# Kernel optimization log

Measured on AMD Instinct MI355X. Metric: run time of the kernel, lower is better.

The kernel has to match this reference:

```python
import jax, jax.numpy as jnp
import numpy as np

GATE_INIT_BIAS = -0.6931471805599453  # -log(2)

def mish(x):
    return x * jnp.tanh(jax.nn.softplus(x))

def setup_inputs() -> dict:
    key = jax.random.key(0)
    ks = jax.random.split(key, 24)
    B = 262144
    x = jax.random.normal(ks[0], (B, 18), dtype=jnp.float32)
    band = jax.random.randint(ks[1], (B,), 0, 9).astype(jnp.float32)
    x = x.at[:, 17].set(band)
    def lin(k, fan_in, shape):
        bound = 1.0 / np.sqrt(fan_in)
        return jax.random.uniform(k, shape, jnp.float32, -bound, bound)
    inp = {
        'x': x,
        # trunk: 15->512->256 (Mish)
        'tw1': lin(ks[2], 15, (15, 512)),  'tb1': lin(ks[3], 15, (512,)),
        'tw2': lin(ks[4], 512, (512, 256)), 'tb2': lin(ks[5], 512, (256,)),
        # 9 band heads: 256->128->1, stacked on leading axis
        'hw1': lin(ks[6], 256, (9, 256, 128)), 'hb1': lin(ks[7], 256, (9, 128)),
        'hw2': lin(ks[8], 128, (9, 128)),      'hb2': lin(ks[9], 128, (9,)),
        # sun scaler head 256->64->1 (final layer zero weight, bias = gate_init_bias)
        'sw1': lin(ks[10], 256, (256, 64)), 'sb1': lin(ks[11], 256, (64,)),
        'sw2': jnp.zeros((64, 1), jnp.float32), 'sb2': jnp.full((1,), GATE_INIT_BIAS, jnp.float32),
        # storm scaler head
        'stw1': lin(ks[12], 256, (256, 64)), 'stb1': lin(ks[13], 256, (64,)),
        'stw2': jnp.zeros((64, 1), jnp.float32), 'stb2': jnp.full((1,), GATE_INIT_BIAS, jnp.float32),
        # monotonic sidecars: 1->8->1, softplus-positivized weights
        'sun_w1': lin(ks[14], 1, (1, 8)),  'sun_b1': lin(ks[15], 1, (8,)),
        'sun_w2': lin(ks[16], 8, (8, 1)),  'sun_b2': lin(ks[17], 8, (1,)),
        'storm_w1': lin(ks[18], 1, (1, 8)), 'storm_b1': lin(ks[19], 1, (8,)),
        'storm_w2': lin(ks[20], 8, (8, 1)), 'storm_b2': lin(ks[21], 8, (1,)),
    }
    return inp

def monotonic_mlp(v, w1, b1, w2, b2):
    # MonotonicMLP: positivity via softplus on weights, tanh hidden activation
    h = jnp.tanh(v @ jax.nn.softplus(w1) + b1)
    return h @ jax.nn.softplus(w2) + b2  # [B,1]

def reference(x, tw1, tb1, tw2, tb2, hw1, hb1, hw2, hb2,
              sw1, sb1, sw2, sb2, stw1, stb1, stw2, stb2,
              sun_w1, sun_b1, sun_w2, sun_b2,
              storm_w1, storm_b1, storm_w2, storm_b2):
    x_deep = x[:, :15]
    x_sfi = x[:, 15:16]
    x_kp = x[:, 16:17]
    band = x[:, 17].astype(jnp.int32)  # [B]

    # trunk
    t = mish(mish(x_deep @ tw1 + tb1) @ tw2 + tb2)  # [B,256]

    # all 9 band heads densely (faithful to original), then gather
    hh = mish(jnp.einsum('bd,kdh->bkh', t, hw1) + hb1)       # [B,9,128]
    all_heads = jnp.einsum('bkh,kh->bk', hh, hw2) + hb2      # [B,9]
    base_snr = jnp.take_along_axis(all_heads, band[:, None], axis=1)  # [B,1]

    sun_logit = mish(t @ sw1 + sb1) @ sw2 + sb2      # [B,1]
    storm_logit = mish(t @ stw1 + stb1) @ stw2 + stb2
    sun_gate = jax.nn.sigmoid(sun_logit)
    storm_gate = jax.nn.sigmoid(storm_logit)

    return base_snr + sun_gate * monotonic_mlp(x_sfi, sun_w1, sun_b1, sun_w2, sun_b2) \
                    + storm_gate * monotonic_mlp(x_kp, storm_w1, storm_b1, storm_w2, storm_b2)
```

## Files before the change

kernel.cpp:

```cpp
#include <hip/hip_runtime.h>
#include <cstdint>

typedef unsigned short u16;
typedef unsigned char u8;
typedef __attribute__((ext_vector_type(8))) __bf16 bf16x8;
typedef __attribute__((ext_vector_type(4))) float f32x4;
typedef __attribute__((ext_vector_type(2))) unsigned u32x2;

#define MFMA16(a, b, c) __builtin_amdgcn_mfma_f32_16x16x32_bf16((a), (b), (c), 0, 0, 0)

__device__ __forceinline__ u16 f2b(float f) {
    union { float f; unsigned u; } v; v.f = f;
    unsigned r = v.u + 0x7fffu + ((v.u >> 16) & 1u);
    return (u16)(r >> 16);
}
__device__ __forceinline__ u16 f2b_hw(float f) {
    union { __bf16 h; u16 u; } cv; cv.h = (__bf16)f; return cv.u;
}
__device__ __forceinline__ float b2f(u16 h) {
    union { unsigned u; float f; } v; v.u = ((unsigned)h) << 16; return v.f;
}
__device__ __forceinline__ unsigned cvt_pk_bf16(float lo, float hi) {
    unsigned r;
    asm("v_cvt_pk_bf16_f32 %0, %1, %2" : "=v"(r) : "v"(lo), "v"(hi));
    return r;
}
__device__ __forceinline__ float fast_rcp(float x) { return __builtin_amdgcn_rcpf(x); }
__device__ __forceinline__ float mish_f(float x) {
    float s = __expf(fminf(x, 40.0f));
    float p = s * (s + 2.0f);
    return x * p * fast_rcp(p + 2.0f);
}
__device__ __forceinline__ float tanh_f(float y) {
    float e = __expf(2.0f * y);
    return 1.0f - 2.0f * fast_rcp(e + 1.0f);
}
__device__ __forceinline__ float sigmoid_f(float y) {
    return fast_rcp(1.0f + __expf(-y));
}
__device__ __forceinline__ float splus(float w) { return log1pf(__expf(w)); }


template <int CTRL>
__device__ __forceinline__ float dpp_add(float v) {
    union { float f; int i; } s, p;
    s.f = v;
    p.i = __builtin_amdgcn_update_dpp(0, s.i, CTRL, 0xf, 0xf, true);
    return v + p.f;
}

#define WS_PERM      0u
#define WS_CNT       1179648u
#define WS_SP        1191936u
#define WS_W1P       1192064u
#define WS_W2F       1224832u
#define WS_HW1F      1486976u
#define WS_SWF       2076800u
#define WS_STWF      2109568u
#define WS_NEEDED    2142336u

#define GFLAG_IDX    2336
#define NSUB         8
#define CAPH         4096
#define REG_BLOCKS   64


__global__ __launch_bounds__(512) void k_pack(const float* __restrict__ x, int B,
                       const float* __restrict__ tw1, const float* __restrict__ tw2,
                       const float* __restrict__ hw1,
                       const float* __restrict__ sw1, const float* __restrict__ stw1,
                       const float* __restrict__ sw2, const float* __restrict__ stw2,
                       const float* __restrict__ sun_w1, const float* __restrict__ sun_w2,
                       const float* __restrict__ storm_w1, const float* __restrict__ storm_w2,
                       u16* __restrict__ W1p, u16* __restrict__ W2f, u16* __restrict__ HWf,
                       u16* __restrict__ SWf, u16* __restrict__ STWf,
                       float* __restrict__ sp, int* __restrict__ cnt,
                       int* __restrict__ perm)
{
    __shared__ int wcnt[8][9];
    __shared__ int wpre[8][9];
    __shared__ int bbase[9];
    __shared__ u8 bL[512];
    const int tid  = threadIdx.x;
    const int lane = tid & 63, wave = tid >> 6;
    const int sub  = blockIdx.x & (NSUB - 1);
    const int i    = blockIdx.x * 512 + tid;

    {
        const size_t ebase = (size_t)blockIdx.x * 512 * 18;
        const float2* xs = (const float2*)(x + ebase);
        const size_t etotal = (size_t)B * 18;
        for (int p = tid; p < 4608; p += 512) {
            if (ebase + (size_t)p * 2 + 1 < etotal) {
                float2 v = xs[p];
                int e0 = p * 2;
                int r0 = e0 / 18, c0 = e0 - r0 * 18;
                if (c0 == 16) bL[r0] = (u8)(int)v.y;
            }
        }
    }
    __syncthreads();

    int band = -1, rank = 0;
    if (i < B) band = (int)bL[tid];
    for (int k = 0; k < 9; ++k) {
        unsigned long long m = __ballot(band == k);
        if (band == k) rank = __popcll(m & ((1ull << lane) - 1ull));
        if (lane == 0) wcnt[wave][k] = __popcll(m);
    }
    __syncthreads();
    if (tid < 9) {
        int run = 0;
        for (int w = 0; w < 8; ++w) { wpre[w][tid] = run; run += wcnt[w][tid]; }
        bbase[tid] = atomicAdd(&cnt[(tid * NSUB + sub) * 32], run);
    }
    __syncthreads();
    if (band >= 0)
        perm[(band * NSUB + sub) * CAPH + bbase[band] + wpre[wave][band] + rank] = i;

    if (blockIdx.x == 0 && tid < 64) {
        bool z = (sw2[tid] == 0.0f) && (stw2[tid] == 0.0f);
        unsigned long long m = __ballot(z);
        if (tid == 0) cnt[GFLAG_IDX] = (m == ~0ull) ? 1 : 0;
    }

    const int gtid = blockIdx.x * 512 + tid;
    if (gtid < 32) {
        const float* srcs[4] = { sun_w1, sun_w2, storm_w1, storm_w2 };
        float w = srcs[gtid >> 3][gtid & 7];
        sp[gtid] = splus(w);
    }
    const int total = 16384 + 131072 + 294912 + 16384 + 16384;
    for (int i2 = gtid; i2 < total; i2 += 512 * 512) {
        int idx = i2;
        if (idx < 16384) {
            int n = idx >> 5, k = idx & 31;
            W1p[idx] = (k < 15) ? f2b(tw1[k * 512 + n]) : (u16)0;
        } else if ((idx -= 16384) < 131072) {
            int tile = idx >> 9, within = idx & 511;
            int lane2 = within >> 3, j = within & 7;
            int nt = tile >> 4, kb = tile & 15;
            int n = nt * 16 + (lane2 & 15);
            int k = kb * 32 + (lane2 >> 4) * 8 + j;
            W2f[idx] = f2b(tw2[k * 256 + n]);
        } else if ((idx -= 131072) < 294912) {
            int g = idx >> 15, r = idx & 32767;
            int tile = r >> 9, within = r & 511;
            int lane2 = within >> 3, j = within & 7;
            int nt = tile >> 3, kb = tile & 7;
            int n = nt * 16 + (lane2 & 15);
            int k = kb * 32 + (lane2 >> 4) * 8 + j;
            HWf[idx] = f2b(hw1[(g * 256 + k) * 128 + n]);
        } else if ((idx -= 294912) < 16384) {
            int tile = idx >> 9, within = idx & 511;
            int lane2 = within >> 3, j = within & 7;
            int nt = tile >> 3, kb = tile & 7;
            int n = nt * 16 + (lane2 & 15);
            int k = kb * 32 + (lane2 >> 4) * 8 + j;
            SWf[idx] = f2b(sw1[k * 64 + n]);
        } else {
            idx -= 16384;
            int tile = idx >> 9, within = idx & 511;
            int lane2 = within >> 3, j = within & 7;
            int nt = tile >> 3, kb = tile & 7;
            int n = nt * 16 + (lane2 & 15);
            int k = kb * 32 + (lane2 >> 4) * 8 + j;
            STWf[idx] = f2b(stw1[k * 64 + n]);
        }
    }
}

__global__ __launch_bounds__(512, 4) void k_main(
                       const float* __restrict__ x,
                       const int* __restrict__ perm,
                       const int* __restrict__ cnt,
                       const u16* __restrict__ W1p, const u16* __restrict__ W2f,
                       const u16* __restrict__ HWf,
                       const u16* __restrict__ SWf, const u16* __restrict__ STWf,
                       const float* __restrict__ tb1, const float* __restrict__ tb2,
                       const float* __restrict__ hb1, const float* __restrict__ hw2,
                       const float* __restrict__ hb2,
                       const float* __restrict__ sb1, const float* __restrict__ sw2,
                       const float* __restrict__ sb2,
                       const float* __restrict__ stb1, const float* __restrict__ stw2,
                       const float* __restrict__ stb2,
                       const float* __restrict__ sp,
                       const float* __restrict__ sun_b1, const float* __restrict__ sun_b2,
                       const float* __restrict__ storm_b1, const float* __restrict__ storm_b2,
                       float* __restrict__ out)
{
    const int region = blockIdx.x >> 6;
    const int loc    = blockIdx.x & 63;
    const int bb     = region >> 3;
    const int nr0    = cnt[region * 32] - loc * 64;
    if (nr0 <= 0) return;
    const int nrows  = nr0 > 64 ? 64 : nr0;
    const int rstart = region * CAPH + loc * 64;
    const int gskip  = cnt[GFLAG_IDX];

    __shared__ union {
        u16 xA[64][32];
        float red[16][64];
    } su;
    __shared__ int rowsL[64];
    __shared__ float sfiL[64], kpL[64];
    __shared__ u16 buf[2][64][136];

    int tid = threadIdx.x;
    int lane = tid & 63, wave = tid >> 6;
    int quad = lane >> 4, l15 = lane & 15;

    if (tid < 64) {
        int r = rstart + (tid < nrows ? tid : 0);
        rowsL[tid] = perm[r];
    }
    for (int i = tid; i < 64 * 32; i += 512) ((u16*)su.xA)[i] = 0;
    __syncthreads();
    for (int i = tid; i < 64 * 18; i += 512) {
        int r = i / 18, c = i - r * 18;
        float v = x[rowsL[r] * 18 + c];
        if (c < 15) su.xA[r][c] = f2b_hw(v);
        else if (c == 15) sfiL[r] = v;
        else if (c == 16) kpL[r] = v;
    }
    __syncthreads();

    bf16x8 ax[4];
#pragma unroll
    for (int mt = 0; mt < 4; ++mt)
        ax[mt] = *(const bf16x8*)&su.xA[mt * 16 + l15][quad * 8];

    f32x4 acc2[2][4] = {};

    for (int c = 0; c < 4; ++c) {
        f32x4 acc1[4] = {};
        {
            int ncol = c * 128 + wave * 16 + l15;
            bf16x8 bw = *(const bf16x8*)&W1p[ncol * 32 + quad * 8];
#pragma unroll
            for (int mt = 0; mt < 4; ++mt)
                acc1[mt] = MFMA16(bw, ax[mt], acc1[mt]);
        }
        u16 (*bufc)[136] = buf[c & 1];
        {
            const f32x4 bias = *(const f32x4*)&tb1[c * 128 + wave * 16 + quad * 4];
#pragma unroll
            for (int mt = 0; mt < 4; ++mt) {
                u32x2 pk;
                pk.x = cvt_pk_bf16(mish_f(acc1[mt][0] + bias[0]),
                                   mish_f(acc1[mt][1] + bias[1]));
                pk.y = cvt_pk_bf16(mish_f(acc1[mt][2] + bias[2]),
                                   mish_f(acc1[mt][3] + bias[3]));
                *(u32x2*)&bufc[mt * 16 + l15][wave * 16 + quad * 4] = pk;
            }
        }
        __syncthreads();
        for (int ks = 0; ks < 4; ++ks) {
            bf16x8 a2[4];
#pragma unroll
            for (int mt = 0; mt < 4; ++mt)
                a2[mt] = *(const bf16x8*)&bufc[mt * 16 + l15][ks * 32 + quad * 8];
            int kb = c * 4 + ks;
#pragma unroll
            for (int ntl = 0; ntl < 2; ++ntl) {
                int nt = wave * 2 + ntl;
                bf16x8 bw = *(const bf16x8*)&W2f[((nt * 16 + kb) << 9) + lane * 8];
#pragma unroll
                for (int mt = 0; mt < 4; ++mt)
                    acc2[ntl][mt] = MFMA16(bw, a2[mt], acc2[ntl][mt]);
            }
        }
    }
    __syncthreads();

    u16 (*tmat)[264] = (u16(*)[264])buf;
#pragma unroll
    for (int ntl = 0; ntl < 2; ++ntl) {
        const int colb = wave * 32 + ntl * 16 + quad * 4;
        const f32x4 bias = *(const f32x4*)&tb2[colb];
#pragma unroll
        for (int mt = 0; mt < 4; ++mt) {
            u32x2 pk;
            pk.x = cvt_pk_bf16(mish_f(acc2[ntl][mt][0] + bias[0]),
                               mish_f(acc2[ntl][mt][1] + bias[1]));
            pk.y = cvt_pk_bf16(mish_f(acc2[ntl][mt][2] + bias[2]),
                               mish_f(acc2[ntl][mt][3] + bias[3]));
            *(u32x2*)&tmat[mt * 16 + l15][colb] = pk;
        }
    }
    __syncthreads();

    f32x4 acch[4] = {}, accg[4] = {};
    const u16* Hw = HWf + bb * 32768;
    const u16* Gw = (wave < 4) ? SWf : STWf;
    int gnt = wave & 3;
    for (int kb = 0; kb < 8; ++kb) {
        bf16x8 a3[4];
#pragma unroll
        for (int mt = 0; mt < 4; ++mt)
            a3[mt] = *(const bf16x8*)&tmat[mt * 16 + l15][kb * 32 + quad * 8];
        bf16x8 bh = *(const bf16x8*)&Hw[((wave * 8 + kb) << 9) + lane * 8];
#pragma unroll
        for (int mt = 0; mt < 4; ++mt)
            acch[mt] = MFMA16(bh, a3[mt], acch[mt]);
        if (!gskip) {
            bf16x8 bg = *(const bf16x8*)&Gw[((gnt * 8 + kb) << 9) + lane * 8];
#pragma unroll
            for (int mt = 0; mt < 4; ++mt)
                accg[mt] = MFMA16(bg, a3[mt], accg[mt]);
        }
    }

    float hpart[4], gpart[4];
    {
        const int colb = wave * 16 + quad * 4;
        const f32x4 hb = *(const f32x4*)&hb1[bb * 128 + colb];
        const f32x4 wv = *(const f32x4*)&hw2[bb * 128 + colb];
#pragma unroll
        for (int mt = 0; mt < 4; ++mt) {
            float s = mish_f(acch[mt][0] + hb[0]) * wv[0];
            s += mish_f(acch[mt][1] + hb[1]) * wv[1];
            s += mish_f(acch[mt][2] + hb[2]) * wv[2];
            s += mish_f(acch[mt][3] + hb[3]) * wv[3];
            hpart[mt] = s;
        }
    }
    if (!gskip) {
        const int nb = gnt * 16 + quad * 4;
        const f32x4 gb = (wave < 4) ? *(const f32x4*)&sb1[nb] : *(const f32x4*)&stb1[nb];
        const f32x4 gw = (wave < 4) ? *(const f32x4*)&sw2[nb] : *(const f32x4*)&stw2[nb];
#pragma unroll
        for (int mt = 0; mt < 4; ++mt) {
            float s = mish_f(accg[mt][0] + gb[0]) * gw[0];
            s += mish_f(accg[mt][1] + gb[1]) * gw[1];
            s += mish_f(accg[mt][2] + gb[2]) * gw[2];
            s += mish_f(accg[mt][3] + gb[3]) * gw[3];
            gpart[mt] = s;
        }
    }
#pragma unroll
    for (int mt = 0; mt < 4; ++mt) {
        float h = hpart[mt];
        h += __shfl_xor(h, 16); h += __shfl_xor(h, 32);
        if (quad == 0) su.red[wave][mt * 16 + l15] = h;
        if (!gskip) {
            float g = gpart[mt];
            g += __shfl_xor(g, 16); g += __shfl_xor(g, 32);
            if (quad == 0) su.red[8 + wave][mt * 16 + l15] = g;
        }
    }
    __syncthreads();

    if (tid < 64 && tid < nrows) {
        int row = tid;
        float head = hb2[bb];
#pragma unroll
        for (int w = 0; w < 8; ++w) head += su.red[w][row];
        float sl = sb2[0], tl = stb2[0];
        if (!gskip) {
#pragma unroll
            for (int w = 0; w < 4; ++w) { sl += su.red[8 + w][row]; tl += su.red[12 + w][row]; }
        }
        float sg = sigmoid_f(sl);
        float tg = sigmoid_f(tl);
        float v1 = sfiL[row], v2 = kpL[row];
        float sun_val = sun_b2[0], storm_val = storm_b2[0];
#pragma unroll
        for (int j = 0; j < 8; ++j) {
            sun_val   += tanh_f(v1 * sp[j]      + sun_b1[j])   * sp[8 + j];
            storm_val += tanh_f(v2 * sp[16 + j] + storm_b1[j]) * sp[24 + j];
        }
        out[rowsL[row]] = head + sg * sun_val + tg * storm_val;
    }
}

__global__ __launch_bounds__(64) void k_simple(
    const float* __restrict__ x,
    const float* __restrict__ tw1, const float* __restrict__ tb1,
    const float* __restrict__ tw2, const float* __restrict__ tb2,
    const float* __restrict__ hw1, const float* __restrict__ hb1,
    const float* __restrict__ hw2, const float* __restrict__ hb2,
    const float* __restrict__ sw1, const float* __restrict__ sb1,
    const float* __restrict__ sw2, const float* __restrict__ sb2,
    const float* __restrict__ stw1, const float* __restrict__ stb1,
    const float* __restrict__ stw2, const float* __restrict__ stb2,
    const float* __restrict__ sun_w1, const float* __restrict__ sun_b1,
    const float* __restrict__ sun_w2, const float* __restrict__ sun_b2,
    const float* __restrict__ storm_w1, const float* __restrict__ storm_b1,
    const float* __restrict__ storm_w2, const float* __restrict__ storm_b2,
    float* __restrict__ out)
{
    __shared__ u16 t_lds[256 * 64];

    const int lane = threadIdx.x;
    const int r = blockIdx.x * 64 + lane;

    float xr[15];
#pragma unroll
    for (int k = 0; k < 15; ++k) xr[k] = x[r * 18 + k];
    const float sfi = x[r * 18 + 15];
    const float kp  = x[r * 18 + 16];
    const int band  = (int)x[r * 18 + 17];

    for (int tc = 0; tc < 4; ++tc) {
        float acc[64];
#pragma unroll
        for (int j = 0; j < 64; ++j) acc[j] = 0.0f;
        for (int n = 0; n < 512; ++n) {
            float p = tb1[n];
#pragma unroll
            for (int k = 0; k < 15; ++k) p += xr[k] * tw1[k * 512 + n];
            const float a1n = mish_f(p);
            const float* w2 = &tw2[n * 256 + tc * 64];
#pragma unroll
            for (int j = 0; j < 64; ++j) acc[j] += a1n * w2[j];
        }
#pragma unroll
        for (int j = 0; j < 64; ++j)
            t_lds[(tc * 64 + j) * 64 + lane] = f2b(mish_f(acc[j] + tb2[tc * 64 + j]));
    }
    __syncthreads();

    float head_val = 0.0f;
    for (int g = 0; g < 9; ++g) {
        float hs = 0.0f;
        for (int hc = 0; hc < 2; ++hc) {
            float pre[64];
#pragma unroll
            for (int j = 0; j < 64; ++j) pre[j] = 0.0f;
            for (int d = 0; d < 256; ++d) {
                const float td = b2f(t_lds[d * 64 + lane]);
                const float* wv = &hw1[g * 32768 + d * 128 + hc * 64];
#pragma unroll
                for (int j = 0; j < 64; ++j) pre[j] += td * wv[j];
            }
#pragma unroll
            for (int j = 0; j < 64; ++j) {
                const int h = hc * 64 + j;
                hs += mish_f(pre[j] + hb1[g * 128 + h]) * hw2[g * 128 + h];
            }
        }
        head_val += (band == g) ? (hs + hb2[g]) : 0.0f;
    }

    float pre_s[64], pre_t[64];
#pragma unroll
    for (int j = 0; j < 64; ++j) { pre_s[j] = 0.0f; pre_t[j] = 0.0f; }
    for (int d = 0; d < 256; ++d) {
        const float td = b2f(t_lds[d * 64 + lane]);
        const float* ws1 = &sw1[d * 64];
        const float* wt1 = &stw1[d * 64];
#pragma unroll
        for (int j = 0; j < 64; ++j) {
            pre_s[j] += td * ws1[j];
            pre_t[j] += td * wt1[j];
        }
    }
    float ls = sb2[0], lt = stb2[0];
#pragma unroll
    for (int j = 0; j < 64; ++j) {
        ls += mish_f(pre_s[j] + sb1[j]) * sw2[j];
        lt += mish_f(pre_t[j] + stb1[j]) * stw2[j];
    }
    const float sg = sigmoid_f(ls);
    const float tg = sigmoid_f(lt);

    float sun_val = sun_b2[0], storm_val = storm_b2[0];
#pragma unroll
    for (int j = 0; j < 8; ++j) {
        sun_val   += tanh_f(sfi * splus(sun_w1[j])  + sun_b1[j])   * splus(sun_w2[j]);
        storm_val += tanh_f(kp * splus(storm_w1[j]) + storm_b1[j]) * splus(storm_w2[j]);
    }

    out[r] = head_val + sg * sun_val + tg * storm_val;
}

extern "C" void kernel_launch(void* const* d_in, const int* in_sizes, int n_in,
                              void* d_out, int out_size, void* d_ws, size_t ws_size,
                              hipStream_t stream) {
    (void)n_in; (void)out_size;
    const float* x        = (const float*)d_in[0];
    const float* tw1      = (const float*)d_in[1];
    const float* tb1      = (const float*)d_in[2];
    const float* tw2      = (const float*)d_in[3];
    const float* tb2      = (const float*)d_in[4];
    const float* hw1      = (const float*)d_in[5];
    const float* hb1      = (const float*)d_in[6];
    const float* hw2      = (const float*)d_in[7];
    const float* hb2      = (const float*)d_in[8];
    const float* sw1      = (const float*)d_in[9];
    const float* sb1      = (const float*)d_in[10];
    const float* sw2      = (const float*)d_in[11];
    const float* sb2      = (const float*)d_in[12];
    const float* stw1     = (const float*)d_in[13];
    const float* stb1     = (const float*)d_in[14];
    const float* stw2     = (const float*)d_in[15];
    const float* stb2     = (const float*)d_in[16];
    const float* sun_w1   = (const float*)d_in[17];
    const float* sun_b1   = (const float*)d_in[18];
    const float* sun_w2   = (const float*)d_in[19];
    const float* sun_b2   = (const float*)d_in[20];
    const float* storm_w1 = (const float*)d_in[21];
    const float* storm_b1 = (const float*)d_in[22];
    const float* storm_w2 = (const float*)d_in[23];
    const float* storm_b2 = (const float*)d_in[24];

    const int B = in_sizes[0] / 18;

    if (ws_size < (size_t)WS_NEEDED) {
        k_simple<<<B / 64, 64, 0, stream>>>(x, tw1, tb1, tw2, tb2, hw1, hb1, hw2, hb2,
                                            sw1, sb1, sw2, sb2, stw1, stb1, stw2, stb2,
                                            sun_w1, sun_b1, sun_w2, sun_b2,
                                            storm_w1, storm_b1, storm_w2, storm_b2,
                                            (float*)d_out);
        return;
    }

    char* ws = (char*)d_ws;
    int*   perm      = (int*)(ws + WS_PERM);
    int*   cnt       = (int*)(ws + WS_CNT);
    float* sp        = (float*)(ws + WS_SP);
    u16*   W1p       = (u16*)(ws + WS_W1P);
    u16*   W2f       = (u16*)(ws + WS_W2F);
    u16*   HWf       = (u16*)(ws + WS_HW1F);
    u16*   SWf       = (u16*)(ws + WS_SWF);
    u16*   STWf      = (u16*)(ws + WS_STWF);

    hipMemsetAsync(cnt, 0, 72 * 32 * sizeof(int), stream);
    k_pack<<<(B + 511) / 512, 512, 0, stream>>>(x, B, tw1, tw2, hw1, sw1, stw1,
                                                sw2, stw2,
                                                sun_w1, sun_w2, storm_w1, storm_w2,
                                                W1p, W2f, HWf, SWf, STWf, sp, cnt, perm);
    k_main<<<72 * REG_BLOCKS, 512, 0, stream>>>(x, perm, cnt,
                                                W1p, W2f, HWf, SWf, STWf,
                                                tb1, tb2, hb1, hw2, hb2,
                                                sb1, sw2, sb2, stb1, stw2, stb2,
                                                sp, sun_b1, sun_b2, storm_b1, storm_b2,
                                                (float*)d_out);
}
```

Baseline: 279.3 us.

## Software-pipeline trunk layer-1 chunks against layer-2 MFMAs and fold biases into accumulators

Computes the first trunk layer chunk before the loop, then inside each chunk iteration issues the next chunk's layer-1 MFMAs and Mish between the two halves of the layer-2 MFMAs. It writes the result into the other LDS buffer, so each chunk needs only one barrier. Biases for all layers are now loaded as initial accumulator values instead of being added before each Mish, and the zeroing loop stores 32-bit words. This is meant to hide transcendental and LDS latency behind matrix work and trim some VALU adds, at the cost of more live registers, which may lower occupancy.

```diff
diff --git a/kernel.cpp b/kernel.cpp
--- a/kernel.cpp
+++ b/kernel.cpp
@@ -214,7 +214,7 @@
         int r = rstart + (tid < nrows ? tid : 0);
         rowsL[tid] = perm[r];
     }
-    for (int i = tid; i < 64 * 32; i += 512) ((u16*)su.xA)[i] = 0;
+    for (int i = tid; i < 64 * 16; i += 512) ((unsigned*)su.xA)[i] = 0u;
     __syncthreads();
     for (int i = tid; i < 64 * 18; i += 512) {
         int r = i / 18, c = i - r * 18;
@@ -230,32 +230,46 @@
     for (int mt = 0; mt < 4; ++mt)
         ax[mt] = *(const bf16x8*)&su.xA[mt * 16 + l15][quad * 8];
 
-    f32x4 acc2[2][4] = {};
-
+    const int colq = wave * 16 + quad * 4;
+
+    f32x4 acc2[2][4];
+#pragma unroll
+    for (int ntl = 0; ntl < 2; ++ntl) {
+        const f32x4 b2v = *(const f32x4*)&tb2[wave * 32 + ntl * 16 + quad * 4];
+#pragma unroll
+        for (int mt = 0; mt < 4; ++mt) acc2[ntl][mt] = b2v;
+    }
+
+    {
+        const f32x4 b1v = *(const f32x4*)&tb1[colq];
+        bf16x8 bw = *(const bf16x8*)&W1p[(wave * 16 + l15) * 32 + quad * 8];
+        f32x4 acc1[4];
+#pragma unroll
+        for (int mt = 0; mt < 4; ++mt) { acc1[mt] = b1v; acc1[mt] = MFMA16(bw, ax[mt], acc1[mt]); }
+#pragma unroll
+        for (int mt = 0; mt < 4; ++mt) {
+            u32x2 pk;
+            pk.x = cvt_pk_bf16(mish_f(acc1[mt][0]), mish_f(acc1[mt][1]));
+            pk.y = cvt_pk_bf16(mish_f(acc1[mt][2]), mish_f(acc1[mt][3]));
+            *(u32x2*)&buf[0][mt * 16 + l15][colq] = pk;
+        }
+    }
+    __syncthreads();
+
+#pragma unroll
     for (int c = 0; c < 4; ++c) {
-        f32x4 acc1[4] = {};
-        {
-            int ncol = c * 128 + wave * 16 + l15;
-            bf16x8 bw = *(const bf16x8*)&W1p[ncol * 32 + quad * 8];
-#pragma unroll
-            for (int mt = 0; mt < 4; ++mt)
-                acc1[mt] = MFMA16(bw, ax[mt], acc1[mt]);
-        }
         u16 (*bufc)[136] = buf[c & 1];
-        {
-            const f32x4 bias = *(const f32x4*)&tb1[c * 128 + wave * 16 + quad * 4];
-#pragma unroll
-            for (int mt = 0; mt < 4; ++mt) {
-                u32x2 pk;
-                pk.x = cvt_pk_bf16(mish_f(acc1[mt][0] + bias[0]),
-                                   mish_f(acc1[mt][1] + bias[1]));
-                pk.y = cvt_pk_bf16(mish_f(acc1[mt][2] + bias[2]),
-                                   mish_f(acc1[mt][3] + bias[3]));
-                *(u32x2*)&bufc[mt * 16 + l15][wave * 16 + quad * 4] = pk;
-            }
-        }
-        __syncthreads();
-        for (int ks = 0; ks < 4; ++ks) {
+        u16 (*bufn)[136] = buf[(c + 1) & 1];
+
+        bf16x8 bwn;
+        f32x4 b1vn;
+        if (c < 3) {
+            b1vn = *(const f32x4*)&tb1[(c + 1) * 128 + colq];
+            bwn = *(const bf16x8*)&W1p[((c + 1) * 128 + wave * 16 + l15) * 32 + quad * 8];
+        }
+
+#pragma unroll
+        for (int ks = 0; ks < 2; ++ks) {
             bf16x8 a2[4];
 #pragma unroll
             for (int mt = 0; mt < 4; ++mt)
@@ -270,30 +284,72 @@
                     acc2[ntl][mt] = MFMA16(bw, a2[mt], acc2[ntl][mt]);
             }
         }
-    }
-    __syncthreads();
+
+        f32x4 acc1n[4];
+        if (c < 3) {
+#pragma unroll
+            for (int mt = 0; mt < 4; ++mt) { acc1n[mt] = b1vn; acc1n[mt] = MFMA16(bwn, ax[mt], acc1n[mt]); }
+        }
+
+#pragma unroll
+        for (int ks = 2; ks < 4; ++ks) {
+            bf16x8 a2[4];
+#pragma unroll
+            for (int mt = 0; mt < 4; ++mt)
+                a2[mt] = *(const bf16x8*)&bufc[mt * 16 + l15][ks * 32 + quad * 8];
+            int kb = c * 4 + ks;
+#pragma unroll
+            for (int ntl = 0; ntl < 2; ++ntl) {
+                int nt = wave * 2 + ntl;
+                bf16x8 bw = *(const bf16x8*)&W2f[((nt * 16 + kb) << 9) + lane * 8];
+#pragma unroll
+                for (int mt = 0; mt < 4; ++mt)
+                    acc2[ntl][mt] = MFMA16(bw, a2[mt], acc2[ntl][mt]);
+            }
+        }
+
+        if (c < 3) {
+#pragma unroll
+            for (int mt = 0; mt < 4; ++mt) {
+                u32x2 pk;
+                pk.x = cvt_pk_bf16(mish_f(acc1n[mt][0]), mish_f(acc1n[mt][1]));
+                pk.y = cvt_pk_bf16(mish_f(acc1n[mt][2]), mish_f(acc1n[mt][3]));
+                *(u32x2*)&bufn[mt * 16 + l15][colq] = pk;
+            }
+        }
+        __syncthreads();
+    }
 
     u16 (*tmat)[264] = (u16(*)[264])buf;
 #pragma unroll
     for (int ntl = 0; ntl < 2; ++ntl) {
         const int colb = wave * 32 + ntl * 16 + quad * 4;
-        const f32x4 bias = *(const f32x4*)&tb2[colb];
 #pragma unroll
         for (int mt = 0; mt < 4; ++mt) {
             u32x2 pk;
-            pk.x = cvt_pk_bf16(mish_f(acc2[ntl][mt][0] + bias[0]),
-                               mish_f(acc2[ntl][mt][1] + bias[1]));
-            pk.y = cvt_pk_bf16(mish_f(acc2[ntl][mt][2] + bias[2]),
-                               mish_f(acc2[ntl][mt][3] + bias[3]));
+            pk.x = cvt_pk_bf16(mish_f(acc2[ntl][mt][0]), mish_f(acc2[ntl][mt][1]));
+            pk.y = cvt_pk_bf16(mish_f(acc2[ntl][mt][2]), mish_f(acc2[ntl][mt][3]));
             *(u32x2*)&tmat[mt * 16 + l15][colb] = pk;
         }
     }
     __syncthreads();
 
-    f32x4 acch[4] = {}, accg[4] = {};
     const u16* Hw = HWf + bb * 32768;
     const u16* Gw = (wave < 4) ? SWf : STWf;
     int gnt = wave & 3;
+    f32x4 acch[4], accg[4];
+    const f32x4 hb = *(const f32x4*)&hb1[bb * 128 + colq];
+#pragma unroll
+    for (int mt = 0; mt < 4; ++mt) acch[mt] = hb;
+    if (!gskip) {
+        const int nb = gnt * 16 + quad * 4;
+        const f32x4 gb = (wave < 4) ? *(const f32x4*)&sb1[nb] : *(const f32x4*)&stb1[nb];
+#pragma unroll
+        for (int mt = 0; mt < 4; ++mt) accg[mt] = gb;
+    } else {
+#pragma unroll
+        for (int mt = 0; mt < 4; ++mt) accg[mt] = (f32x4){0.f, 0.f, 0.f, 0.f};
+    }
     for (int kb = 0; kb < 8; ++kb) {
         bf16x8 a3[4];
 #pragma unroll
@@ -313,28 +369,25 @@
 
     float hpart[4], gpart[4];
     {
-        const int colb = wave * 16 + quad * 4;
-        const f32x4 hb = *(const f32x4*)&hb1[bb * 128 + colb];
-        const f32x4 wv = *(const f32x4*)&hw2[bb * 128 + colb];
+        const f32x4 wv = *(const f32x4*)&hw2[bb * 128 + colq];
 #pragma unroll
         for (int mt = 0; mt < 4; ++mt) {
-            float s = mish_f(acch[mt][0] + hb[0]) * wv[0];
-            s += mish_f(acch[mt][1] + hb[1]) * wv[1];
-            s += mish_f(acch[mt][2] + hb[2]) * wv[2];
-            s += mish_f(acch[mt][3] + hb[3]) * wv[3];
+            float s = mish_f(acch[mt][0]) * wv[0];
+            s += mish_f(acch[mt][1]) * wv[1];
+            s += mish_f(acch[mt][2]) * wv[2];
+            s += mish_f(acch[mt][3]) * wv[3];
             hpart[mt] = s;
         }
     }
     if (!gskip) {
         const int nb = gnt * 16 + quad * 4;
-        const f32x4 gb = (wave < 4) ? *(const f32x4*)&sb1[nb] : *(const f32x4*)&stb1[nb];
         const f32x4 gw = (wave < 4) ? *(const f32x4*)&sw2[nb] : *(const f32x4*)&stw2[nb];
 #pragma unroll
         for (int mt = 0; mt < 4; ++mt) {
-            float s = mish_f(accg[mt][0] + gb[0]) * gw[0];
-            s += mish_f(accg[mt][1] + gb[1]) * gw[1];
-            s += mish_f(accg[mt][2] + gb[2]) * gw[2];
-            s += mish_f(accg[mt][3] + gb[3]) * gw[3];
+            float s = mish_f(accg[mt][0]) * gw[0];
+            s += mish_f(accg[mt][1]) * gw[1];
+            s += mish_f(accg[mt][2]) * gw[2];
+            s += mish_f(accg[mt][3]) * gw[3];
             gpart[mt] = s;
         }
     }
```

Result: no change. 282.8 us (+1.2%).

## Double rows per block to 128 and fold biases into MFMA accumulators

Applied to the files above, without the earlier changes.

Each block now processes 128 rows instead of 64, with half as many blocks per region, so every weight fragment loaded from global memory feeds eight MFMAs instead of four. Bias vectors now initialise the accumulators, which removes the separate bias adds before each Mish. The wave reductions are also written into the per-row reduction buffer directly. In exchange, registers and LDS per block roughly double (buf grows to about 70KB), which may lower occupancy, and partially filled tail blocks waste more work.

```diff
diff --git a/kernel.cpp b/kernel.cpp
--- a/kernel.cpp
+++ b/kernel.cpp
@@ -62,7 +62,8 @@
 #define GFLAG_IDX    2336
 #define NSUB         8
 #define CAPH         4096
-#define REG_BLOCKS   64
+#define ROWS_PB      128
+#define REG_BLOCKS   32
 
 
 __global__ __launch_bounds__(512) void k_pack(const float* __restrict__ x, int B,
@@ -189,34 +190,34 @@
                        const float* __restrict__ storm_b1, const float* __restrict__ storm_b2,
                        float* __restrict__ out)
 {
-    const int region = blockIdx.x >> 6;
-    const int loc    = blockIdx.x & 63;
+    const int region = blockIdx.x >> 5;
+    const int loc    = blockIdx.x & 31;
     const int bb     = region >> 3;
-    const int nr0    = cnt[region * 32] - loc * 64;
+    const int nr0    = cnt[region * 32] - loc * ROWS_PB;
     if (nr0 <= 0) return;
-    const int nrows  = nr0 > 64 ? 64 : nr0;
-    const int rstart = region * CAPH + loc * 64;
+    const int nrows  = nr0 > ROWS_PB ? ROWS_PB : nr0;
+    const int rstart = region * CAPH + loc * ROWS_PB;
     const int gskip  = cnt[GFLAG_IDX];
 
     __shared__ union {
-        u16 xA[64][32];
-        float red[16][64];
+        u16 xA[128][32];
+        float red[16][128];
     } su;
-    __shared__ int rowsL[64];
-    __shared__ float sfiL[64], kpL[64];
-    __shared__ u16 buf[2][64][136];
+    __shared__ int rowsL[128];
+    __shared__ float sfiL[128], kpL[128];
+    __shared__ u16 buf[2][128][136];
 
     int tid = threadIdx.x;
     int lane = tid & 63, wave = tid >> 6;
     int quad = lane >> 4, l15 = lane & 15;
 
-    if (tid < 64) {
+    if (tid < 128) {
         int r = rstart + (tid < nrows ? tid : 0);
         rowsL[tid] = perm[r];
     }
-    for (int i = tid; i < 64 * 32; i += 512) ((u16*)su.xA)[i] = 0;
-    __syncthreads();
-    for (int i = tid; i < 64 * 18; i += 512) {
+    for (int i = tid; i < 128 * 16; i += 512) ((unsigned*)su.xA)[i] = 0u;
+    __syncthreads();
+    for (int i = tid; i < 128 * 18; i += 512) {
         int r = i / 18, c = i - r * 18;
         float v = x[rowsL[r] * 18 + c];
         if (c < 15) su.xA[r][c] = f2b_hw(v);
@@ -225,40 +226,38 @@
     }
     __syncthreads();
 
-    bf16x8 ax[4];
-#pragma unroll
-    for (int mt = 0; mt < 4; ++mt)
-        ax[mt] = *(const bf16x8*)&su.xA[mt * 16 + l15][quad * 8];
-
-    f32x4 acc2[2][4] = {};
+    const int colq = wave * 16 + quad * 4;
+
+    f32x4 acc2[2][8];
+#pragma unroll
+    for (int ntl = 0; ntl < 2; ++ntl) {
+        const f32x4 b2v = *(const f32x4*)&tb2[wave * 32 + ntl * 16 + quad * 4];
+#pragma unroll
+        for (int mt = 0; mt < 8; ++mt) acc2[ntl][mt] = b2v;
+    }
 
     for (int c = 0; c < 4; ++c) {
-        f32x4 acc1[4] = {};
-        {
-            int ncol = c * 128 + wave * 16 + l15;
-            bf16x8 bw = *(const bf16x8*)&W1p[ncol * 32 + quad * 8];
-#pragma unroll
-            for (int mt = 0; mt < 4; ++mt)
-                acc1[mt] = MFMA16(bw, ax[mt], acc1[mt]);
-        }
         u16 (*bufc)[136] = buf[c & 1];
         {
-            const f32x4 bias = *(const f32x4*)&tb1[c * 128 + wave * 16 + quad * 4];
-#pragma unroll
-            for (int mt = 0; mt < 4; ++mt) {
+            const f32x4 b1v = *(const f32x4*)&tb1[c * 128 + colq];
+            bf16x8 bw = *(const bf16x8*)&W1p[(c * 128 + wave * 16 + l15) * 32 + quad * 8];
+#pragma unroll
+            for (int mt = 0; mt < 8; ++mt) {
+                bf16x8 ax = *(const bf16x8*)&su.xA[mt * 16 + l15][quad * 8];
+                f32x4 a1 = b1v;
+                a1 = MFMA16(bw, ax, a1);
                 u32x2 pk;
-                pk.x = cvt_pk_bf16(mish_f(acc1[mt][0] + bias[0]),
-                                   mish_f(acc1[mt][1] + bias[1]));
-                pk.y = cvt_pk_bf16(mish_f(acc1[mt][2] + bias[2]),
-                                   mish_f(acc1[mt][3] + bias[3]));
-                *(u32x2*)&bufc[mt * 16 + l15][wave * 16 + quad * 4] = pk;
+                pk.x = cvt_pk_bf16(mish_f(a1[0]), mish_f(a1[1]));
+                pk.y = cvt_pk_bf16(mish_f(a1[2]), mish_f(a1[3]));
+                *(u32x2*)&bufc[mt * 16 + l15][colq] = pk;
             }
         }
         __syncthreads();
+#pragma unroll
         for (int ks = 0; ks < 4; ++ks) {
-            bf16x8 a2[4];
-#pragma unroll
-            for (int mt = 0; mt < 4; ++mt)
+            bf16x8 a2[8];
+#pragma unroll
+            for (int mt = 0; mt < 8; ++mt)
                 a2[mt] = *(const bf16x8*)&bufc[mt * 16 + l15][ks * 32 + quad * 8];
             int kb = c * 4 + ks;
 #pragma unroll
@@ -266,7 +265,7 @@
                 int nt = wave * 2 + ntl;
                 bf16x8 bw = *(const bf16x8*)&W2f[((nt * 16 + kb) << 9) + lane * 8];
 #pragma unroll
-                for (int mt = 0; mt < 4; ++mt)
+                for (int mt = 0; mt < 8; ++mt)
                     acc2[ntl][mt] = MFMA16(bw, a2[mt], acc2[ntl][mt]);
             }
         }
@@ -277,81 +276,76 @@
 #pragma unroll
     for (int ntl = 0; ntl < 2; ++ntl) {
         const int colb = wave * 32 + ntl * 16 + quad * 4;
-        const f32x4 bias = *(const f32x4*)&tb2[colb];
-#pragma unroll
-        for (int mt = 0; mt < 4; ++mt) {
+#pragma unroll
+        for (int mt = 0; mt < 8; ++mt) {
             u32x2 pk;
-            pk.x = cvt_pk_bf16(mish_f(acc2[ntl][mt][0] + bias[0]),
-                               mish_f(acc2[ntl][mt][1] + bias[1]));
-            pk.y = cvt_pk_bf16(mish_f(acc2[ntl][mt][2] + bias[2]),
-                               mish_f(acc2[ntl][mt][3] + bias[3]));
+            pk.x = cvt_pk_bf16(mish_f(acc2[ntl][mt][0]), mish_f(acc2[ntl][mt][1]));
+            pk.y = cvt_pk_bf16(mish_f(acc2[ntl][mt][2]), mish_f(acc2[ntl][mt][3]));
             *(u32x2*)&tmat[mt * 16 + l15][colb] = pk;
         }
     }
     __syncthreads();
 
-    f32x4 acch[4] = {}, accg[4] = {};
     const u16* Hw = HWf + bb * 32768;
     const u16* Gw = (wave < 4) ? SWf : STWf;
     int gnt = wave & 3;
+    f32x4 acch[8], accg[8];
+    {
+        const f32x4 hb = *(const f32x4*)&hb1[bb * 128 + colq];
+#pragma unroll
+        for (int mt = 0; mt < 8; ++mt) acch[mt] = hb;
+    }
+    if (!gskip) {
+        const int nb = gnt * 16 + quad * 4;
+        const f32x4 gb = (wave < 4) ? *(const f32x4*)&sb1[nb] : *(const f32x4*)&stb1[nb];
+#pragma unroll
+        for (int mt = 0; mt < 8; ++mt) accg[mt] = gb;
+    }
     for (int kb = 0; kb < 8; ++kb) {
-        bf16x8 a3[4];
-#pragma unroll
-        for (int mt = 0; mt < 4; ++mt)
+        bf16x8 a3[8];
+#pragma unroll
+        for (int mt = 0; mt < 8; ++mt)
             a3[mt] = *(const bf16x8*)&tmat[mt * 16 + l15][kb * 32 + quad * 8];
         bf16x8 bh = *(const bf16x8*)&Hw[((wave * 8 + kb) << 9) + lane * 8];
 #pragma unroll
-        for (int mt = 0; mt < 4; ++mt)
+        for (int mt = 0; mt < 8; ++mt)
             acch[mt] = MFMA16(bh, a3[mt], acch[mt]);
         if (!gskip) {
             bf16x8 bg = *(const bf16x8*)&Gw[((gnt * 8 + kb) << 9) + lane * 8];
 #pragma unroll
-            for (int mt = 0; mt < 4; ++mt)
+            for (int mt = 0; mt < 8; ++mt)
                 accg[mt] = MFMA16(bg, a3[mt], accg[mt]);
         }
     }
 
-    float hpart[4], gpart[4];
     {
-        const int colb = wave * 16 + quad * 4;
-        const f32x4 hb = *(const f32x4*)&hb1[bb * 128 + colb];
-        const f32x4 wv = *(const f32x4*)&hw2[bb * 128 + colb];
-#pragma unroll
-        for (int mt = 0; mt < 4; ++mt) {
-            float s = mish_f(acch[mt][0] + hb[0]) * wv[0];
-            s += mish_f(acch[mt][1] + hb[1]) * wv[1];
-            s += mish_f(acch[mt][2] + hb[2]) * wv[2];
-            s += mish_f(acch[mt][3] + hb[3]) * wv[3];
-            hpart[mt] = s;
+        const f32x4 wv = *(const f32x4*)&hw2[bb * 128 + colq];
+#pragma unroll
+        for (int mt = 0; mt < 8; ++mt) {
+            float s = mish_f(acch[mt][0]) * wv[0];
+            s += mish_f(acch[mt][1]) * wv[1];
+            s += mish_f(acch[mt][2]) * wv[2];
+            s += mish_f(acch[mt][3]) * wv[3];
+            s += __shfl_xor(s, 16); s += __shfl_xor(s, 32);
+            if (quad == 0) su.red[wave][mt * 16 + l15] = s;
         }
     }
     if (!gskip) {
         const int nb = gnt * 16 + quad * 4;
-        const f32x4 gb = (wave < 4) ? *(const f32x4*)&sb1[nb] : *(const f32x4*)&stb1[nb];
         const f32x4 gw = (wave < 4) ? *(const f32x4*)&sw2[nb] : *(const f32x4*)&stw2[nb];
 #pragma unroll
-        for (int mt = 0; mt < 4; ++mt) {
-            float s = mish_f(accg[mt][0] + gb[0]) * gw[0];
-            s += mish_f(accg[mt][1] + gb[1]) * gw[1];
-            s += mish_f(accg[mt][2] + gb[2]) * gw[2];
-            s += mish_f(accg[mt][3] + gb[3]) * gw[3];
-            gpart[mt] = s;
-        }
-    }
-#pragma unroll
-    for (int mt = 0; mt < 4; ++mt) {
-        float h = hpart[mt];
-        h += __shfl_xor(h, 16); h += __shfl_xor(h, 32);
-        if (quad == 0) su.red[wave][mt * 16 + l15] = h;
-        if (!gskip) {
-            float g = gpart[mt];
-            g += __shfl_xor(g, 16); g += __shfl_xor(g, 32);
-            if (quad == 0) su.red[8 + wave][mt * 16 + l15] = g;
-        }
-    }
-    __syncthreads();
-
-    if (tid < 64 && tid < nrows) {
+        for (int mt = 0; mt < 8; ++mt) {
+            float s = mish_f(accg[mt][0]) * gw[0];
+            s += mish_f(accg[mt][1]) * gw[1];
+            s += mish_f(accg[mt][2]) * gw[2];
+            s += mish_f(accg[mt][3]) * gw[3];
+            s += __shfl_xor(s, 16); s += __shfl_xor(s, 32);
+            if (quad == 0) su.red[8 + wave][mt * 16 + l15] = s;
+        }
+    }
+    __syncthreads();
+
+    if (tid < 128 && tid < nrows) {
         int row = tid;
         float head = hb2[bb];
 #pragma unroll
```

Result: slower. 369.3 us (+32.2%).
